# Performance work log

Measured on AMD Instinct MI355X. Metric: run time of the kernel, lower is better.

## Reference

```python
import jax, jax.numpy as jnp
import numpy as np

N_NODES = 50000
D_FEAT = 512
N_EDGES = 100000


def setup_inputs() -> dict:
    key = jax.random.key(0)
    k0, k1, k2, k3, k4 = jax.random.split(key, 5)
    return {
        "out": jax.random.normal(k0, (N_NODES, D_FEAT), dtype=jnp.float32),
        "pos_src": jax.random.randint(k1, (N_EDGES,), 0, N_NODES),
        "pos_dst": jax.random.randint(k2, (N_EDGES,), 0, N_NODES),
        "neg_src": jax.random.randint(k3, (N_EDGES,), 0, N_NODES),
        "neg_dst": jax.random.randint(k4, (N_EDGES,), 0, N_NODES),
    }


def _edge_scores(out, src, dst):
    # per-edge u . v dot product (fn.u_dot_v): gather + reduce over feature dim
    return jnp.sum(out[src] * out[dst], axis=-1)  # [E]


def reference(out, pos_src, pos_dst, neg_src, neg_dst):
    pos_score = _edge_scores(out, pos_src, pos_dst)  # [E_pos]
    neg_score = _edge_scores(out, neg_src, neg_dst)  # [E_neg]
    score = jnp.concatenate([pos_score, neg_score])  # [E_pos + E_neg]
    label = jnp.concatenate([
        jnp.ones(pos_score.shape[0], dtype=score.dtype),
        jnp.zeros(neg_score.shape[0], dtype=score.dtype),
    ])
    # numerically-stable binary_cross_entropy_with_logits, mean reduction
    loss = jnp.mean(
        jnp.maximum(score, 0.0) - score * label + jnp.log1p(jnp.exp(-jnp.abs(score)))
    )
    return loss
```

## Files before the change

kernel.cpp:

```cpp
#include <hip/hip_runtime.h>
#include <math.h>

#define D_FEAT 512
#define WAVES_PER_BLOCK 4
#define NBLOCKS 2048

__global__ __launch_bounds__(256) void edge_bce_partial(
    const float* __restrict__ feat,
    const int* __restrict__ pos_src, const int* __restrict__ pos_dst,
    const int* __restrict__ neg_src, const int* __restrict__ neg_dst,
    int n_edges, double* __restrict__ partials)
{
    const int lane = threadIdx.x & 63;
    const int wave = threadIdx.x >> 6;
    const int wave_global = blockIdx.x * WAVES_PER_BLOCK + wave;
    const int n_waves = gridDim.x * WAVES_PER_BLOCK;
    const int total = 2 * n_edges;

    double acc = 0.0;
    for (int e = wave_global; e < total; e += n_waves) {
        int src, dst; float label;
        if (e < n_edges) {
            src = pos_src[e];           dst = pos_dst[e];           label = 1.0f;
        } else {
            src = neg_src[e - n_edges]; dst = neg_dst[e - n_edges]; label = 0.0f;
        }
        const float4* u = (const float4*)(feat + (size_t)src * D_FEAT);
        const float4* v = (const float4*)(feat + (size_t)dst * D_FEAT);
        float4 u0 = u[lane], u1 = u[lane + 64];
        float4 v0 = v[lane], v1 = v[lane + 64];
        float d = u0.x*v0.x + u0.y*v0.y + u0.z*v0.z + u0.w*v0.w
                + u1.x*v1.x + u1.y*v1.y + u1.z*v1.z + u1.w*v1.w;
        #pragma unroll
        for (int off = 32; off; off >>= 1) d += __shfl_xor(d, off, 64);
        if (lane == 0) {
            float s = d;
            float t = fmaxf(s, 0.0f) - s * label + log1pf(expf(-fabsf(s)));
            acc += (double)t;
        }
    }

    __shared__ double wsum[WAVES_PER_BLOCK];
    if (lane == 0) wsum[wave] = acc;
    __syncthreads();
    if (threadIdx.x == 0) {
        double b = 0.0;
        #pragma unroll
        for (int i = 0; i < WAVES_PER_BLOCK; ++i) b += wsum[i];
        partials[blockIdx.x] = b;
    }
}

__global__ __launch_bounds__(256) void reduce_partials(
    const double* __restrict__ partials, int n, float* __restrict__ out_scalar,
    double inv_count)
{
    double a = 0.0;
    for (int i = threadIdx.x; i < n; i += 256) a += partials[i];
    #pragma unroll
    for (int off = 32; off; off >>= 1) a += __shfl_xor(a, off, 64);
    __shared__ double w[4];
    const int lane = threadIdx.x & 63, wv = threadIdx.x >> 6;
    if (lane == 0) w[wv] = a;
    __syncthreads();
    if (threadIdx.x == 0) {
        out_scalar[0] = (float)((w[0] + w[1] + w[2] + w[3]) * inv_count);
    }
}

extern "C" void kernel_launch(void* const* d_in, const int* in_sizes, int n_in,
                              void* d_out, int out_size, void* d_ws, size_t ws_size,
                              hipStream_t stream) {
    const float* feat    = (const float*)d_in[0];
    const int*   pos_src = (const int*)d_in[1];
    const int*   pos_dst = (const int*)d_in[2];
    const int*   neg_src = (const int*)d_in[3];
    const int*   neg_dst = (const int*)d_in[4];
    const int n_edges = in_sizes[1];

    double* partials = (double*)d_ws;
    float*  out      = (float*)d_out;

    edge_bce_partial<<<NBLOCKS, 256, 0, stream>>>(
        feat, pos_src, pos_dst, neg_src, neg_dst, n_edges, partials);
    reduce_partials<<<1, 256, 0, stream>>>(
        partials, NBLOCKS, out, 1.0 / (2.0 * (double)n_edges));
}
```

Before: 245.6 us.

## Convert feature table to bf16 and gather half-precision rows per half-wave

```diff
diff --git a/kernel.cpp b/kernel.cpp
--- a/kernel.cpp
+++ b/kernel.cpp
@@ -4,6 +4,91 @@
 #define D_FEAT 512
 #define WAVES_PER_BLOCK 4
 #define NBLOCKS 2048
+
+typedef unsigned int uint32;
+
+__device__ __forceinline__ float bf_lo(uint32 w) { return __uint_as_float(w << 16); }
+__device__ __forceinline__ float bf_hi(uint32 w) { return __uint_as_float(w & 0xffff0000u); }
+
+__global__ __launch_bounds__(256) void convert_bf16(
+    const float* __restrict__ feat, uint32* __restrict__ bt, int n8)
+{
+    const float4* f4 = (const float4*)feat;
+    const int stride = gridDim.x * blockDim.x;
+    for (int i = blockIdx.x * blockDim.x + threadIdx.x; i < n8; i += stride) {
+        float4 a = f4[2*i], b = f4[2*i + 1];
+        const float src[8] = {a.x, a.y, a.z, a.w, b.x, b.y, b.z, b.w};
+        uint32 w[8];
+        #pragma unroll
+        for (int k = 0; k < 8; ++k) {
+            uint32 u = __float_as_uint(src[k]);
+            u = u + 0x7fffu + ((u >> 16) & 1u);
+            w[k] = u >> 16;
+        }
+        uint4 o;
+        o.x = w[0] | (w[1] << 16);
+        o.y = w[2] | (w[3] << 16);
+        o.z = w[4] | (w[5] << 16);
+        o.w = w[6] | (w[7] << 16);
+        ((uint4*)bt)[i] = o;
+    }
+}
+
+__global__ __launch_bounds__(256) void edge_bce_bf16(
+    const uint32* __restrict__ bt,
+    const int* __restrict__ pos_src, const int* __restrict__ pos_dst,
+    const int* __restrict__ neg_src, const int* __restrict__ neg_dst,
+    int n_edges, double* __restrict__ partials)
+{
+    const int lane = threadIdx.x & 63;
+    const int sub  = lane & 31;
+    const int half = lane >> 5;
+    const int wave = threadIdx.x >> 6;
+    const int slot = (blockIdx.x * WAVES_PER_BLOCK + wave) * 2 + half;
+    const int n_slots = gridDim.x * WAVES_PER_BLOCK * 2;
+    const int total = 2 * n_edges;
+
+    double acc = 0.0;
+    for (int e = slot; e < total; e += n_slots) {
+        const bool pos = e < n_edges;
+        const int  i   = pos ? e : e - n_edges;
+        const int  src = pos ? pos_src[i] : neg_src[i];
+        const int  dst = pos ? pos_dst[i] : neg_dst[i];
+        const uint4* u = (const uint4*)(bt + (size_t)src * (D_FEAT / 2));
+        const uint4* v = (const uint4*)(bt + (size_t)dst * (D_FEAT / 2));
+        uint4 u0 = u[sub], u1 = u[sub + 32];
+        uint4 v0 = v[sub], v1 = v[sub + 32];
+
+        float d =
+              bf_lo(u0.x)*bf_lo(v0.x) + bf_hi(u0.x)*bf_hi(v0.x)
+            + bf_lo(u0.y)*bf_lo(v0.y) + bf_hi(u0.y)*bf_hi(v0.y)
+            + bf_lo(u0.z)*bf_lo(v0.z) + bf_hi(u0.z)*bf_hi(v0.z)
+            + bf_lo(u0.w)*bf_lo(v0.w) + bf_hi(u0.w)*bf_hi(v0.w)
+            + bf_lo(u1.x)*bf_lo(v1.x) + bf_hi(u1.x)*bf_hi(v1.x)
+            + bf_lo(u1.y)*bf_lo(v1.y) + bf_hi(u1.y)*bf_hi(v1.y)
+            + bf_lo(u1.z)*bf_lo(v1.z) + bf_hi(u1.z)*bf_hi(v1.z)
+            + bf_lo(u1.w)*bf_lo(v1.w) + bf_hi(u1.w)*bf_hi(v1.w);
+
+        #pragma unroll
+        for (int off = 1; off <= 16; off <<= 1) d += __shfl_xor(d, off, 64);
+
+        if (sub == 0) {
+            float s = d;
+            float t = fmaxf(s, 0.0f) - (pos ? s : 0.0f) + log1pf(expf(-fabsf(s)));
+            acc += (double)t;
+        }
+    }
+
+    __shared__ double wsum[WAVES_PER_BLOCK * 2];
+    if (sub == 0) wsum[wave * 2 + half] = acc;
+    __syncthreads();
+    if (threadIdx.x == 0) {
+        double b = 0.0;
+        #pragma unroll
+        for (int i = 0; i < WAVES_PER_BLOCK * 2; ++i) b += wsum[i];
+        partials[blockIdx.x] = b;
+    }
+}
 
 __global__ __launch_bounds__(256) void edge_bce_partial(
     const float* __restrict__ feat,
@@ -20,11 +105,8 @@
     double acc = 0.0;
     for (int e = wave_global; e < total; e += n_waves) {
         int src, dst; float label;
-        if (e < n_edges) {
-            src = pos_src[e];           dst = pos_dst[e];           label = 1.0f;
-        } else {
-            src = neg_src[e - n_edges]; dst = neg_dst[e - n_edges]; label = 0.0f;
-        }
+        if (e < n_edges) { src = pos_src[e]; dst = pos_dst[e]; label = 1.0f; }
+        else { src = neg_src[e - n_edges]; dst = neg_dst[e - n_edges]; label = 0.0f; }
         const float4* u = (const float4*)(feat + (size_t)src * D_FEAT);
         const float4* v = (const float4*)(feat + (size_t)dst * D_FEAT);
         float4 u0 = u[lane], u1 = u[lane + 64];
@@ -35,11 +117,9 @@
         for (int off = 32; off; off >>= 1) d += __shfl_xor(d, off, 64);
         if (lane == 0) {
             float s = d;
-            float t = fmaxf(s, 0.0f) - s * label + log1pf(expf(-fabsf(s)));
-            acc += (double)t;
+            acc += (double)(fmaxf(s, 0.0f) - s * label + log1pf(expf(-fabsf(s))));
         }
     }
-
     __shared__ double wsum[WAVES_PER_BLOCK];
     if (lane == 0) wsum[wave] = acc;
     __syncthreads();
@@ -77,12 +157,24 @@
     const int*   neg_src = (const int*)d_in[3];
     const int*   neg_dst = (const int*)d_in[4];
     const int n_edges = in_sizes[1];
+    const int n_feat  = in_sizes[0];
 
     double* partials = (double*)d_ws;
     float*  out      = (float*)d_out;
 
-    edge_bce_partial<<<NBLOCKS, 256, 0, stream>>>(
-        feat, pos_src, pos_dst, neg_src, neg_dst, n_edges, partials);
+    const size_t bt_off   = (size_t)NBLOCKS * sizeof(double);
+    const size_t bt_bytes = (size_t)n_feat * 2;
+    const bool   use_bf16 = ws_size >= bt_off + bt_bytes;
+
+    if (use_bf16) {
+        uint32* bt = (uint32*)((char*)d_ws + bt_off);
+        convert_bf16<<<NBLOCKS, 256, 0, stream>>>(feat, bt, n_feat / 8);
+        edge_bce_bf16<<<NBLOCKS, 256, 0, stream>>>(
+            bt, pos_src, pos_dst, neg_src, neg_dst, n_edges, partials);
+    } else {
+        edge_bce_partial<<<NBLOCKS, 256, 0, stream>>>(
+            feat, pos_src, pos_dst, neg_src, neg_dst, n_edges, partials);
+    }
     reduce_partials<<<1, 256, 0, stream>>>(
         partials, NBLOCKS, out, 1.0 / (2.0 * (double)n_edges));
 }
```

Result: faster. 220.8 us (-10.1%).
